# Performance work log

Measured on AMD Instinct MI355X. Metric: run time of the kernel, lower is better.

Reference implementation:

```python
import jax, jax.numpy as jnp
import numpy as np

HID = 512
HEADS = 8
DK = HID // HEADS


def setup_inputs() -> dict:
    key = jax.random.key(0)
    ks = jax.random.split(key, 11)
    B, Nq, Nk = 2, 4096, 4096
    s = 1.0 / np.sqrt(HID)
    inp = {
        "query": jax.random.normal(ks[0], (B, Nq, HID), jnp.float32),
        "key": jax.random.normal(ks[1], (B, Nk, HID), jnp.float32),
        "value": jax.random.normal(ks[2], (B, Nk, HID), jnp.float32),
        "Wq": jax.random.normal(ks[3], (HID, HID), jnp.float32) * s,
        "bq": jnp.zeros((HID,), jnp.float32),
        "Wk": jax.random.normal(ks[4], (HID, HID), jnp.float32) * s,
        "bk": jnp.zeros((HID,), jnp.float32),
        "Wv": jax.random.normal(ks[5], (HID, HID), jnp.float32) * s,
        "bv": jnp.zeros((HID,), jnp.float32),
        "Wo": jax.random.normal(ks[6], (HID, HID), jnp.float32) * s,
        "bo": jnp.zeros((HID,), jnp.float32),
    }
    return inp


def reference(query, key, value, Wq, bq, Wk, bk, Wv, bv, Wo, bo):
    B, Nq, _ = query.shape
    Nk = key.shape[1]
    # torch Linear: x @ W.T + b
    Q = (query @ Wq.T + bq).reshape(B, Nq, HEADS, DK).transpose(0, 2, 1, 3)  # (B,H,Nq,dk)
    K = (key @ Wk.T + bk).reshape(B, Nk, HEADS, DK).transpose(0, 2, 1, 3)    # (B,H,Nk,dk)
    V = (value @ Wv.T + bv).reshape(B, Nk, HEADS, DK).transpose(0, 2, 1, 3)  # (B,H,Nk,dk)
    scale = 1.0 / jnp.sqrt(jnp.asarray(DK, query.dtype))
    scores = jnp.einsum("bhqd,bhkd->bhqk", Q, K) * scale  # (B,H,Nq,Nk)
    attn = jax.nn.softmax(scores, axis=-1)
    # dropout is identity in eval/inference mode (deterministic reference)
    context = jnp.einsum("bhqk,bhkd->bhqd", attn, V)  # (B,H,Nq,dk)
    context = context.transpose(0, 2, 1, 3).reshape(B, Nq, HID)
    out = context @ Wo.T + bo
    return out, attn
```

## Files before the change

### kernel.cpp

```cpp
#include <hip/hip_runtime.h>
#include <hip/hip_bf16.h>

#define NB   2
#define NH   8
#define NSEQ 4096
#define DKH  64
#define HD   512

typedef unsigned short u16;
typedef unsigned int   u32;
typedef short s16x8 __attribute__((ext_vector_type(8)));
typedef u16   u16x8 __attribute__((ext_vector_type(8)));
typedef u16   u16x4 __attribute__((ext_vector_type(4)));
typedef u32   u32x2 __attribute__((ext_vector_type(2)));
typedef float f32x4 __attribute__((ext_vector_type(4)));

#define L2E 1.4426950408889634f

static __device__ __forceinline__ u16 f2bf(float f) {
    u32 u = __builtin_bit_cast(u32, f);
    u32 r = (u + 0x7fffu + ((u >> 16) & 1u)) >> 16;
    return (u16)r;
}
static __device__ __forceinline__ f32x4 mm16(s16x8 a, s16x8 b, f32x4 c) {
    return __builtin_amdgcn_mfma_f32_16x16x32_bf16(a, b, c, 0, 0, 0);
}
static __device__ __forceinline__ s16x8 ld8(const u16* p) {
    return __builtin_bit_cast(s16x8, *(const u16x8*)p);
}
static __device__ __forceinline__ void bar_sync() {
    __builtin_amdgcn_sched_barrier(0);
    asm volatile("s_waitcnt lgkmcnt(0)" ::: "memory");
    __builtin_amdgcn_sched_barrier(0);
    __builtin_amdgcn_s_barrier();
    __builtin_amdgcn_sched_barrier(0);
}

__launch_bounds__(512, 2)
__global__ void qkv_proj_kernel(const float* __restrict__ Xq, const float* __restrict__ Xk,
                                const float* __restrict__ Xv,
                                const float* __restrict__ Wq, const float* __restrict__ Wk,
                                const float* __restrict__ Wv,
                                const float* __restrict__ bq, const float* __restrict__ bk,
                                const float* __restrict__ bv,
                                u16* __restrict__ Yq, u16* __restrict__ Yk,
                                u16* __restrict__ Yv)
{
    __shared__ u16 xh[128][40], wh[128][40];
    __shared__ u16 st[9216];
    const int t = threadIdx.x;
    const int lane = t & 63, wave = t >> 6;
    const int lg = lane >> 4, lr = lane & 15;
    const int wr = (wave >> 2) * 64, wc = (wave & 3) * 32;
    const int m0 = blockIdx.x * 128, n0 = blockIdx.y * 128;

    const float* X; const float* W; const float* B; u16* Y; float scale; int mode;
    if (blockIdx.z == 0)      { X = Xq; W = Wq; B = bq; Y = Yq; scale = 0.125f; mode = 0; }
    else if (blockIdx.z == 1) { X = Xk; W = Wk; B = bk; Y = Yk; scale = 1.0f;   mode = 0; }
    else                      { X = Xv; W = Wv; B = bv; Y = Yv; scale = 1.0f;   mode = 1; }

    f32x4 acc[4][2] = {};

    for (int k0 = 0; k0 < HD; k0 += 32) {
        #pragma unroll
        for (int i = 0; i < 2; i++) {
            int idx = t + i * 512;
            int r = idx >> 3, c = (idx & 7) * 4;
            float4 v = *(const float4*)(X + (size_t)(m0 + r) * HD + k0 + c);
            u16x4 hv; hv[0] = f2bf(v.x); hv[1] = f2bf(v.y); hv[2] = f2bf(v.z); hv[3] = f2bf(v.w);
            *(u16x4*)&xh[r][c] = hv;
            float4 w = *(const float4*)(W + (size_t)(n0 + r) * HD + k0 + c);
            u16x4 gv; gv[0] = f2bf(w.x); gv[1] = f2bf(w.y); gv[2] = f2bf(w.z); gv[3] = f2bf(w.w);
            *(u16x4*)&wh[r][c] = gv;
        }
        __syncthreads();
        const int kk = lg * 8;
        s16x8 ah[4], bh[2];
        #pragma unroll
        for (int f = 0; f < 4; f++) ah[f] = ld8(&xh[wr + f * 16 + lr][kk]);
        #pragma unroll
        for (int f = 0; f < 2; f++) bh[f] = ld8(&wh[wc + f * 16 + lr][kk]);
        #pragma unroll
        for (int m = 0; m < 4; m++)
            #pragma unroll
            for (int n = 0; n < 2; n++)
                acc[m][n] = mm16(ah[m], bh[n], acc[m][n]);
        __syncthreads();
    }

    float bv2[2];
    #pragma unroll
    for (int n = 0; n < 2; n++) bv2[n] = B[n0 + wc + n * 16 + lr];

    const int mych = (wave & 3) >> 1;
    const int wcl  = wc & 63;

    #pragma unroll
    for (int ch = 0; ch < 2; ch++) {
        if (mych == ch) {
            #pragma unroll
            for (int m = 0; m < 4; m++)
                #pragma unroll
                for (int n = 0; n < 2; n++) {
                    int c = wcl + n * 16 + lr;
                    #pragma unroll
                    for (int j = 0; j < 4; j++) {
                        int r = wr + m * 16 + lg * 4 + j;
                        u16 hv = f2bf((acc[m][n][j] + bv2[n]) * scale);
                        if (mode == 0) st[r * 72 + c]  = hv;
                        else           st[c * 136 + r] = hv;
                    }
                }
        }
        __syncthreads();
        const int hh = (n0 >> 6) + ch;
        if (mode == 0) {
            #pragma unroll
            for (int i = 0; i < 2; i++) {
                int flat = t + i * 512;
                int r = flat >> 3, dc = (flat & 7) * 8;
                int row = m0 + r, b = row >> 12, nn = row & (NSEQ - 1);
                size_t o = (((size_t)(b * NH + hh) * NSEQ) + nn) * DKH + dc;
                *(u16x8*)(Y + o) = *(const u16x8*)&st[r * 72 + dc];
            }
        } else {
            #pragma unroll
            for (int i = 0; i < 2; i++) {
                int flat = t + i * 512;
                int c = flat >> 4, rc = (flat & 15) * 8;
                int row = m0 + rc, b = row >> 12, nn = row & (NSEQ - 1);
                size_t o = ((size_t)(b * NH + hh) * DKH + c) * (size_t)NSEQ + nn;
                *(u16x8*)(Y + o) = *(const u16x8*)&st[c * 136 + rc];
            }
        }
        if (ch == 0) __syncthreads();
    }
}

static __device__ __forceinline__ void swz_bh_q(int& bh, int& qblk) {
    int f = blockIdx.x + 32 * blockIdx.y;
    int r = f & 7, q = f >> 3;
    bh = 2 * r + (q >> 5);
    qblk = q & 31;
}

#define NT (NSEQ / 64)
#define PP 68

__launch_bounds__(256, 3)
__global__ void attn_kernel(const u16* __restrict__ Qh, const u16* __restrict__ Kh,
                            const u16* __restrict__ Vt,
                            float* __restrict__ attn, u16* __restrict__ ctx)
{
    __shared__ u16 kh[2][64][72], vt[2][64][72];
    __shared__ u16 plds[4][32][PP];
    const int t = threadIdx.x, lane = t & 63, wave = t >> 6;
    const int lg = lane >> 4, lr = lane & 15;
    int bh, qblk; swz_bh_q(bh, qblk);
    const int q0 = qblk * 128 + wave * 32;
    const size_t nbase = (size_t)bh * NSEQ;

    const int sr = t >> 3;
    const int sc = (t & 7) * 8;
    const u16* gK = Kh + nbase * DKH + (size_t)sr * DKH + sc;
    const u16* gV = Vt + ((size_t)bh * DKH + sr) * NSEQ + sc;

    s16x8 qh[2][2];
    #pragma unroll
    for (int qi = 0; qi < 2; qi++)
        #pragma unroll
        for (int ds = 0; ds < 2; ds++)
            qh[qi][ds] = ld8(Qh + (nbase + q0 + qi * 16 + lr) * DKH + ds * 32 + lg * 8);

    float sums[2] = {0.f, 0.f};
    {
        *(u16x8*)&kh[0][sr][sc]      = *(const u16x8*)(gK);
        *(u16x8*)&kh[0][sr + 32][sc] = *(const u16x8*)(gK + (size_t)32 * DKH);
        bar_sync();
        for (int tt = 0; tt < NT; tt++) {
            const int cur = tt & 1, nxt = cur ^ 1;
            u16x8 pk0, pk1;
            if (tt + 1 < NT) {
                pk0 = *(const u16x8*)(gK + (size_t)(tt * 64 + 64) * DKH);
                pk1 = *(const u16x8*)(gK + (size_t)(tt * 64 + 96) * DKH);
            }
            f32x4 S[2][4] = {};
            __builtin_amdgcn_s_setprio(1);
            #pragma unroll
            for (int ds = 0; ds < 2; ds++) {
                s16x8 bf[4];
                #pragma unroll
                for (int kf = 0; kf < 4; kf++)
                    bf[kf] = ld8(&kh[cur][kf * 16 + lr][ds * 32 + lg * 8]);
                #pragma unroll
                for (int qi = 0; qi < 2; qi++)
                    #pragma unroll
                    for (int kf = 0; kf < 4; kf++)
                        S[qi][kf] = mm16(bf[kf], qh[qi][ds], S[qi][kf]);
            }
            __builtin_amdgcn_s_setprio(0);
            #pragma unroll
            for (int qi = 0; qi < 2; qi++)
                #pragma unroll
                for (int kf = 0; kf < 4; kf++)
                    #pragma unroll
                    for (int j = 0; j < 4; j++)
                        sums[qi] += __builtin_amdgcn_exp2f(S[qi][kf][j] * L2E);
            if (tt + 1 < NT) {
                *(u16x8*)&kh[nxt][sr][sc]      = pk0;
                *(u16x8*)&kh[nxt][sr + 32][sc] = pk1;
            }
            bar_sync();
        }
    }
    #pragma unroll
    for (int qi = 0; qi < 2; qi++) {
        sums[qi] += __shfl_xor(sums[qi], 16, 64);
        sums[qi] += __shfl_xor(sums[qi], 32, 64);
    }

    float lrl[2];
    float* aptr[2];
    #pragma unroll
    for (int qi = 0; qi < 2; qi++) {
        lrl[qi] = -__builtin_amdgcn_logf(sums[qi]);
        aptr[qi] = attn + (nbase + q0 + qi * 16 + lr) * (size_t)NSEQ + lg * 4;
    }

    #pragma unroll
    for (int i = 0; i < 2; i++) {
        int r = sr + i * 32;
        *(u16x8*)&kh[0][r][sc] = *(const u16x8*)(gK + (size_t)(i * 32) * DKH);
        *(u16x8*)&vt[0][r][sc] = *(const u16x8*)(gV + (size_t)(i * 32) * NSEQ);
    }
    bar_sync();

    f32x4 O[2][4] = {};
    for (int tt = 0; tt < NT; tt++) {
        const int cur = tt & 1, nxt = cur ^ 1;
        const int k0 = tt * 64;

        u16x8 pk[2], pv[2];
        if (tt + 1 < NT) {
            #pragma unroll
            for (int i = 0; i < 2; i++) {
                pk[i] = *(const u16x8*)(gK + (size_t)(k0 + 64 + i * 32) * DKH);
                pv[i] = *(const u16x8*)(gV + (size_t)(i * 32) * NSEQ + k0 + 64);
            }
        }

        f32x4 S[2][4] = {};
        __builtin_amdgcn_s_setprio(1);
        #pragma unroll
        for (int ds = 0; ds < 2; ds++) {
            s16x8 bkh[4];
            #pragma unroll
            for (int kf = 0; kf < 4; kf++)
                bkh[kf] = ld8(&kh[cur][kf * 16 + lr][ds * 32 + lg * 8]);
            #pragma unroll
            for (int qi = 0; qi < 2; qi++)
                #pragma unroll
                for (int kf = 0; kf < 4; kf++)
                    S[qi][kf] = mm16(bkh[kf], qh[qi][ds], S[qi][kf]);
        }
        __builtin_amdgcn_s_setprio(0);

        #pragma unroll
        for (int qi = 0; qi < 2; qi++)
            #pragma unroll
            for (int kf = 0; kf < 4; kf++) {
                f32x4 p;
                #pragma unroll
                for (int j = 0; j < 4; j++)
                    p[j] = __builtin_amdgcn_exp2f(fmaf(S[qi][kf][j], L2E, lrl[qi]));
                *(f32x4*)(aptr[qi] + kf * 16) = p;
                u32x2 pk2;
                pk2[0] = (u32)f2bf(p[0]) | ((u32)f2bf(p[1]) << 16);
                pk2[1] = (u32)f2bf(p[2]) | ((u32)f2bf(p[3]) << 16);
                *(u32x2*)&plds[wave][qi * 16 + lr][kf * 16 + lg * 4] = pk2;
            }

        __builtin_amdgcn_wave_barrier();

        __builtin_amdgcn_s_setprio(1);
        #pragma unroll
        for (int ks = 0; ks < 2; ks++) {
            s16x8 pa[2], vb[4];
            #pragma unroll
            for (int qi = 0; qi < 2; qi++)
                pa[qi] = ld8(&plds[wave][qi * 16 + lr][ks * 32 + lg * 8]);
            #pragma unroll
            for (int df = 0; df < 4; df++)
                vb[df] = ld8(&vt[cur][df * 16 + lr][ks * 32 + lg * 8]);
            #pragma unroll
            for (int qi = 0; qi < 2; qi++)
                #pragma unroll
                for (int df = 0; df < 4; df++)
                    O[qi][df] = mm16(pa[qi], vb[df], O[qi][df]);
        }
        __builtin_amdgcn_s_setprio(0);

        if (tt + 1 < NT) {
            #pragma unroll
            for (int i = 0; i < 2; i++) {
                int r = sr + i * 32;
                *(u16x8*)&kh[nxt][r][sc] = pk[i];
                *(u16x8*)&vt[nxt][r][sc] = pv[i];
            }
        }
        aptr[0] += 64;
        aptr[1] += 64;
        bar_sync();
    }

    const int b = bh >> 3, h = bh & 7;
    #pragma unroll
    for (int qi = 0; qi < 2; qi++)
        #pragma unroll
        for (int df = 0; df < 4; df++)
            #pragma unroll
            for (int j = 0; j < 4; j++) {
                int n = q0 + qi * 16 + lg * 4 + j;
                int col = h * 64 + df * 16 + lr;
                ctx[((size_t)b * NSEQ + n) * HD + col] = f2bf(O[qi][df][j]);
            }
}

__launch_bounds__(512, 2)
__global__ void outproj_kernel(const u16* __restrict__ Xc, const float* __restrict__ W,
                               const float* __restrict__ bias, float* __restrict__ out)
{
    __shared__ u16 xh[128][72], wh[128][72];
    const int t = threadIdx.x, lane = t & 63, wave = t >> 6;
    const int lg = lane >> 4, lr = lane & 15;
    const int wr = (wave >> 2) * 64, wc = (wave & 3) * 32;
    const int m0 = blockIdx.x * 128, n0 = blockIdx.y * 128;

    f32x4 acc[4][2] = {};
    for (int k0 = 0; k0 < HD; k0 += 64) {
        #pragma unroll
        for (int i = 0; i < 2; i++) {
            int idx = t + i * 512;
            int r = idx >> 3, c = (idx & 7) * 8;
            *(u16x8*)&xh[r][c] = *(const u16x8*)(Xc + (size_t)(m0 + r) * HD + k0 + c);
        }
        #pragma unroll
        for (int i = 0; i < 4; i++) {
            int idx = t + i * 512;
            int r = idx >> 4, c = (idx & 15) * 4;
            float4 v = *(const float4*)(W + (size_t)(n0 + r) * HD + k0 + c);
            u16x4 gv; gv[0] = f2bf(v.x); gv[1] = f2bf(v.y); gv[2] = f2bf(v.z); gv[3] = f2bf(v.w);
            *(u16x4*)&wh[r][c] = gv;
        }
        __syncthreads();
        #pragma unroll
        for (int ks = 0; ks < 2; ks++) {
            s16x8 af[4], bf[2];
            int kk = ks * 32 + lg * 8;
            #pragma unroll
            for (int f = 0; f < 4; f++) af[f] = ld8(&xh[wr + f * 16 + lr][kk]);
            #pragma unroll
            for (int f = 0; f < 2; f++) bf[f] = ld8(&wh[wc + f * 16 + lr][kk]);
            #pragma unroll
            for (int m = 0; m < 4; m++)
                #pragma unroll
                for (int n = 0; n < 2; n++)
                    acc[m][n] = mm16(af[m], bf[n], acc[m][n]);
        }
        __syncthreads();
    }
    #pragma unroll
    for (int m = 0; m < 4; m++)
        #pragma unroll
        for (int n = 0; n < 2; n++) {
            int col = n0 + wc + n * 16 + lr;
            float bv = bias[col];
            #pragma unroll
            for (int j = 0; j < 4; j++) {
                int row = m0 + wr + m * 16 + lg * 4 + j;
                out[(size_t)row * HD + col] = acc[m][n][j] + bv;
            }
        }
}

extern "C" void kernel_launch(void* const* d_in, const int* in_sizes, int n_in,
                              void* d_out, int out_size, void* d_ws, size_t ws_size,
                              hipStream_t stream)
{
    const float* query = (const float*)d_in[0];
    const float* key   = (const float*)d_in[1];
    const float* value = (const float*)d_in[2];
    const float* Wq = (const float*)d_in[3];
    const float* bq = (const float*)d_in[4];
    const float* Wk = (const float*)d_in[5];
    const float* bk = (const float*)d_in[6];
    const float* Wv = (const float*)d_in[7];
    const float* bv = (const float*)d_in[8];
    const float* Wo = (const float*)d_in[9];
    const float* bo = (const float*)d_in[10];

    float* out  = (float*)d_out;
    float* attn = out + (size_t)NB * NSEQ * HD;

    const size_t E = (size_t)NB * NH * NSEQ * DKH;
    u16* qhi = (u16*)d_ws;
    u16* khi = qhi + E;
    u16* vt  = khi + E;
    u16* ctx = vt + E;

    qkv_proj_kernel<<<dim3(64, 4, 3), dim3(512), 0, stream>>>(
        query, key, value, Wq, Wk, Wv, bq, bk, bv, qhi, khi, vt);
    attn_kernel<<<dim3(32, 16), dim3(256), 0, stream>>>(qhi, khi, vt, attn, ctx);
    outproj_kernel<<<dim3(64, 4), dim3(512), 0, stream>>>(ctx, Wo, bo, out);
}
```

Before: 387.5 us.

## Split attention block into 8 waves of 16 query rows each

The attention kernel now runs 512 threads per block, with each wave handling 16 query rows instead of 32, and K/V tiles loaded cooperatively with one vector per thread. The goal is more waves in flight to hide latency of the memory-bound attn writes and exp work, and lower per-thread register pressure. In exchange each K/V tile loaded into LDS is reused by fewer rows per wave, so there are more LDS reads per MFMA, and the block-wide barriers now cover more waves.

```diff
diff --git a/kernel.cpp b/kernel.cpp
--- a/kernel.cpp
+++ b/kernel.cpp
@@ -147,17 +147,17 @@
 #define NT (NSEQ / 64)
 #define PP 68
 
-__launch_bounds__(256, 3)
+__launch_bounds__(512, 4)
 __global__ void attn_kernel(const u16* __restrict__ Qh, const u16* __restrict__ Kh,
                             const u16* __restrict__ Vt,
                             float* __restrict__ attn, u16* __restrict__ ctx)
 {
-    __shared__ u16 kh[2][64][72], vt[2][64][72];
-    __shared__ u16 plds[4][32][PP];
+    __shared__ u16 kbuf[4][64][72];
+    __shared__ u16 plds[8][16][PP];
     const int t = threadIdx.x, lane = t & 63, wave = t >> 6;
     const int lg = lane >> 4, lr = lane & 15;
     int bh, qblk; swz_bh_q(bh, qblk);
-    const int q0 = qblk * 128 + wave * 32;
+    const int q0 = qblk * 128 + wave * 16;
     const size_t nbase = (size_t)bh * NSEQ;
 
     const int sr = t >> 3;
@@ -165,165 +165,124 @@
     const u16* gK = Kh + nbase * DKH + (size_t)sr * DKH + sc;
     const u16* gV = Vt + ((size_t)bh * DKH + sr) * NSEQ + sc;
 
-    s16x8 qh[2][2];
-    #pragma unroll
-    for (int qi = 0; qi < 2; qi++)
-        #pragma unroll
-        for (int ds = 0; ds < 2; ds++)
-            qh[qi][ds] = ld8(Qh + (nbase + q0 + qi * 16 + lr) * DKH + ds * 32 + lg * 8);
-
-    float sums[2] = {0.f, 0.f};
+    s16x8 qh[2];
+    #pragma unroll
+    for (int ds = 0; ds < 2; ds++)
+        qh[ds] = ld8(Qh + (nbase + q0 + lr) * DKH + ds * 32 + lg * 8);
+
+    float sums = 0.f;
     {
-        *(u16x8*)&kh[0][sr][sc]      = *(const u16x8*)(gK);
-        *(u16x8*)&kh[0][sr + 32][sc] = *(const u16x8*)(gK + (size_t)32 * DKH);
+        *(u16x8*)&kbuf[0][sr][sc] = *(const u16x8*)(gK);
         bar_sync();
         for (int tt = 0; tt < NT; tt++) {
             const int cur = tt & 1, nxt = cur ^ 1;
-            u16x8 pk0, pk1;
-            if (tt + 1 < NT) {
+            u16x8 pk0;
+            if (tt + 1 < NT)
                 pk0 = *(const u16x8*)(gK + (size_t)(tt * 64 + 64) * DKH);
-                pk1 = *(const u16x8*)(gK + (size_t)(tt * 64 + 96) * DKH);
-            }
-            f32x4 S[2][4] = {};
+            f32x4 S[4] = {};
             __builtin_amdgcn_s_setprio(1);
             #pragma unroll
             for (int ds = 0; ds < 2; ds++) {
                 s16x8 bf[4];
                 #pragma unroll
                 for (int kf = 0; kf < 4; kf++)
-                    bf[kf] = ld8(&kh[cur][kf * 16 + lr][ds * 32 + lg * 8]);
-                #pragma unroll
-                for (int qi = 0; qi < 2; qi++)
-                    #pragma unroll
-                    for (int kf = 0; kf < 4; kf++)
-                        S[qi][kf] = mm16(bf[kf], qh[qi][ds], S[qi][kf]);
+                    bf[kf] = ld8(&kbuf[cur][kf * 16 + lr][ds * 32 + lg * 8]);
+                #pragma unroll
+                for (int kf = 0; kf < 4; kf++)
+                    S[kf] = mm16(bf[kf], qh[ds], S[kf]);
             }
             __builtin_amdgcn_s_setprio(0);
             #pragma unroll
-            for (int qi = 0; qi < 2; qi++)
-                #pragma unroll
-                for (int kf = 0; kf < 4; kf++)
-                    #pragma unroll
-                    for (int j = 0; j < 4; j++)
-                        sums[qi] += __builtin_amdgcn_exp2f(S[qi][kf][j] * L2E);
-            if (tt + 1 < NT) {
-                *(u16x8*)&kh[nxt][sr][sc]      = pk0;
-                *(u16x8*)&kh[nxt][sr + 32][sc] = pk1;
-            }
+            for (int kf = 0; kf < 4; kf++)
+                #pragma unroll
+                for (int j = 0; j < 4; j++)
+                    sums += __builtin_amdgcn_exp2f(S[kf][j] * L2E);
+            if (tt + 1 < NT)
+                *(u16x8*)&kbuf[nxt][sr][sc] = pk0;
             bar_sync();
         }
     }
-    #pragma unroll
-    for (int qi = 0; qi < 2; qi++) {
-        sums[qi] += __shfl_xor(sums[qi], 16, 64);
-        sums[qi] += __shfl_xor(sums[qi], 32, 64);
-    }
-
-    float lrl[2];
-    float* aptr[2];
-    #pragma unroll
-    for (int qi = 0; qi < 2; qi++) {
-        lrl[qi] = -__builtin_amdgcn_logf(sums[qi]);
-        aptr[qi] = attn + (nbase + q0 + qi * 16 + lr) * (size_t)NSEQ + lg * 4;
-    }
-
-    #pragma unroll
-    for (int i = 0; i < 2; i++) {
-        int r = sr + i * 32;
-        *(u16x8*)&kh[0][r][sc] = *(const u16x8*)(gK + (size_t)(i * 32) * DKH);
-        *(u16x8*)&vt[0][r][sc] = *(const u16x8*)(gV + (size_t)(i * 32) * NSEQ);
-    }
+    sums += __shfl_xor(sums, 16, 64);
+    sums += __shfl_xor(sums, 32, 64);
+
+    const float lrl = -__builtin_amdgcn_logf(sums);
+    float* aptr = attn + (nbase + q0 + lr) * (size_t)NSEQ + lg * 4;
+
+    *(u16x8*)&kbuf[0][sr][sc] = *(const u16x8*)(gK);
+    *(u16x8*)&kbuf[2][sr][sc] = *(const u16x8*)(gV);
     bar_sync();
 
-    f32x4 O[2][4] = {};
+    f32x4 O[4] = {};
     for (int tt = 0; tt < NT; tt++) {
         const int cur = tt & 1, nxt = cur ^ 1;
         const int k0 = tt * 64;
 
-        u16x8 pk[2], pv[2];
+        u16x8 pk0, pv0;
         if (tt + 1 < NT) {
-            #pragma unroll
-            for (int i = 0; i < 2; i++) {
-                pk[i] = *(const u16x8*)(gK + (size_t)(k0 + 64 + i * 32) * DKH);
-                pv[i] = *(const u16x8*)(gV + (size_t)(i * 32) * NSEQ + k0 + 64);
-            }
-        }
-
-        f32x4 S[2][4] = {};
+            pk0 = *(const u16x8*)(gK + (size_t)(k0 + 64) * DKH);
+            pv0 = *(const u16x8*)(gV + k0 + 64);
+        }
+
+        f32x4 S[4] = {};
         __builtin_amdgcn_s_setprio(1);
         #pragma unroll
         for (int ds = 0; ds < 2; ds++) {
             s16x8 bkh[4];
             #pragma unroll
             for (int kf = 0; kf < 4; kf++)
-                bkh[kf] = ld8(&kh[cur][kf * 16 + lr][ds * 32 + lg * 8]);
-            #pragma unroll
-            for (int qi = 0; qi < 2; qi++)
-                #pragma unroll
-                for (int kf = 0; kf < 4; kf++)
-                    S[qi][kf] = mm16(bkh[kf], qh[qi][ds], S[qi][kf]);
+                bkh[kf] = ld8(&kbuf[cur][kf * 16 + lr][ds * 32 + lg * 8]);
+            #pragma unroll
+            for (int kf = 0; kf < 4; kf++)
+                S[kf] = mm16(bkh[kf], qh[ds], S[kf]);
         }
         __builtin_amdgcn_s_setprio(0);
 
         #pragma unroll
-        for (int qi = 0; qi < 2; qi++)
-            #pragma unroll
-            for (int kf = 0; kf < 4; kf++) {
-                f32x4 p;
-                #pragma unroll
-                for (int j = 0; j < 4; j++)
-                    p[j] = __builtin_amdgcn_exp2f(fmaf(S[qi][kf][j], L2E, lrl[qi]));
-                *(f32x4*)(aptr[qi] + kf * 16) = p;
-                u32x2 pk2;
-                pk2[0] = (u32)f2bf(p[0]) | ((u32)f2bf(p[1]) << 16);
-                pk2[1] = (u32)f2bf(p[2]) | ((u32)f2bf(p[3]) << 16);
-                *(u32x2*)&plds[wave][qi * 16 + lr][kf * 16 + lg * 4] = pk2;
-            }
+        for (int kf = 0; kf < 4; kf++) {
+            f32x4 p;
+            #pragma unroll
+            for (int j = 0; j < 4; j++)
+                p[j] = __builtin_amdgcn_exp2f(fmaf(S[kf][j], L2E, lrl));
+            *(f32x4*)(aptr + kf * 16) = p;
+            u32x2 pk2;
+            pk2[0] = (u32)f2bf(p[0]) | ((u32)f2bf(p[1]) << 16);
+            pk2[1] = (u32)f2bf(p[2]) | ((u32)f2bf(p[3]) << 16);
+            *(u32x2*)&plds[wave][lr][kf * 16 + lg * 4] = pk2;
+        }
 
         __builtin_amdgcn_wave_barrier();
 
         __builtin_amdgcn_s_setprio(1);
         #pragma unroll
         for (int ks = 0; ks < 2; ks++) {
-            s16x8 pa[2], vb[4];
-            #pragma unroll
-            for (int qi = 0; qi < 2; qi++)
-                pa[qi] = ld8(&plds[wave][qi * 16 + lr][ks * 32 + lg * 8]);
+            s16x8 pa, vb[4];
+            pa = ld8(&plds[wave][lr][ks * 32 + lg * 8]);
             #pragma unroll
             for (int df = 0; df < 4; df++)
-                vb[df] = ld8(&vt[cur][df * 16 + lr][ks * 32 + lg * 8]);
-            #pragma unroll
-            for (int qi = 0; qi < 2; qi++)
-                #pragma unroll
-                for (int df = 0; df < 4; df++)
-                    O[qi][df] = mm16(pa[qi], vb[df], O[qi][df]);
+                vb[df] = ld8(&kbuf[2 + cur][df * 16 + lr][ks * 32 + lg * 8]);
+            #pragma unroll
+            for (int df = 0; df < 4; df++)
+                O[df] = mm16(pa, vb[df], O[df]);
         }
         __builtin_amdgcn_s_setprio(0);
 
         if (tt + 1 < NT) {
-            #pragma unroll
-            for (int i = 0; i < 2; i++) {
-                int r = sr + i * 32;
-                *(u16x8*)&kh[nxt][r][sc] = pk[i];
-                *(u16x8*)&vt[nxt][r][sc] = pv[i];
-            }
-        }
-        aptr[0] += 64;
-        aptr[1] += 64;
+            *(u16x8*)&kbuf[nxt][sr][sc]     = pk0;
+            *(u16x8*)&kbuf[2 + nxt][sr][sc] = pv0;
+        }
+        aptr += 64;
         bar_sync();
     }
 
     const int b = bh >> 3, h = bh & 7;
     #pragma unroll
-    for (int qi = 0; qi < 2; qi++)
-        #pragma unroll
-        for (int df = 0; df < 4; df++)
-            #pragma unroll
-            for (int j = 0; j < 4; j++) {
-                int n = q0 + qi * 16 + lg * 4 + j;
-                int col = h * 64 + df * 16 + lr;
-                ctx[((size_t)b * NSEQ + n) * HD + col] = f2bf(O[qi][df][j]);
-            }
+    for (int df = 0; df < 4; df++)
+        #pragma unroll
+        for (int j = 0; j < 4; j++) {
+            int n = q0 + lg * 4 + j;
+            int col = h * 64 + df * 16 + lr;
+            ctx[((size_t)b * NSEQ + n) * HD + col] = f2bf(O[df][j]);
+        }
 }
 
 __launch_bounds__(512, 2)
@@ -410,6 +369,6 @@
 
     qkv_proj_kernel<<<dim3(64, 4, 3), dim3(512), 0, stream>>>(
         query, key, value, Wq, Wk, Wv, bq, bk, bv, qhi, khi, vt);
-    attn_kernel<<<dim3(32, 16), dim3(256), 0, stream>>>(qhi, khi, vt, attn, ctx);
+    attn_kernel<<<dim3(32, 16), dim3(512), 0, stream>>>(qhi, khi, vt, attn, ctx);
     outproj_kernel<<<dim3(64, 4), dim3(512), 0, stream>>>(ctx, Wo, bo, out);
 }
```

Result: slower. 470.2 us (+21.3%).
